# Kernel tuning notes

Measured on AMD Instinct MI355X. Metric: run time of the kernel, lower is better.

Reference implementation:

```python
import jax, jax.numpy as jnp
import numpy as np

N = 100000
E = 800000
IN_DIM = 128
H = 4
D = 32
HD = H * D  # 128
EPS = 1e-5
NEG_SLOPE = 0.2


def setup_inputs() -> dict:
    key = jax.random.key(0)
    ks = jax.random.split(key, 12)
    feat = jax.random.normal(ks[0], (N, IN_DIM), dtype=jnp.float32)
    src = jax.random.randint(ks[1], (E,), 0, N)
    dst = jax.random.randint(ks[2], (E,), 0, N)
    s = 1.0 / np.sqrt(IN_DIM)
    W_src = jax.random.uniform(ks[3], (HD, IN_DIM), jnp.float32, -s, s)
    b_src = jax.random.uniform(ks[4], (HD,), jnp.float32, -s, s)
    attn_l = jax.random.normal(ks[5], (1, H, D), dtype=jnp.float32) * np.sqrt(2.0 / (H * D + 1)) * np.sqrt(2.0)
    attn_r = jax.random.normal(ks[6], (1, H, D), dtype=jnp.float32) * np.sqrt(2.0 / (H * D + 1)) * np.sqrt(2.0)
    W_skip = jax.random.uniform(ks[7], (HD, IN_DIM), jnp.float32, -s, s)
    b_skip = jax.random.uniform(ks[8], (HD,), jnp.float32, -s, s)
    sg = 1.0 / np.sqrt(3 * HD)
    W_gate = jax.random.uniform(ks[9], (1, 3 * HD), jnp.float32, -sg, sg)
    b_gate = jax.random.uniform(ks[10], (1,), jnp.float32, -sg, sg)
    ln_g = jnp.ones((HD,), jnp.float32)
    ln_b = jnp.zeros((HD,), jnp.float32)
    prelu_a = jnp.full((1,), 0.25, jnp.float32)
    return {"feat": feat, "src": src, "dst": dst, "W_src": W_src, "b_src": b_src,
            "attn_l": attn_l, "attn_r": attn_r, "W_skip": W_skip, "b_skip": b_skip,
            "W_gate": W_gate, "b_gate": b_gate, "ln_g": ln_g, "ln_b": ln_b,
            "prelu_a": prelu_a}


def reference(feat, src, dst, W_src, b_src, attn_l, attn_r, W_skip, b_skip,
              W_gate, b_gate, ln_g, ln_b, prelu_a):
    # node projection -> [N, H, D]
    feat_src = (feat @ W_src.T + b_src).reshape(N, H, D)
    el = jnp.sum(feat_src * attn_l, axis=-1)  # [N, H]
    er = jnp.sum(feat_src * attn_r, axis=-1)  # [N, H]
    # per-edge logits with leaky relu
    e = el[src] + er[dst]                      # [E, H]
    e = jnp.where(e >= 0, e, NEG_SLOPE * e)
    # edge softmax over incoming edges of each dst node
    emax = jax.ops.segment_max(e, dst, num_segments=N)   # [N, H]
    ex = jnp.exp(e - emax[dst])                          # [E, H]
    esum = jax.ops.segment_sum(ex, dst, num_segments=N)  # [N, H]
    a = ex / esum[dst]                                   # [E, H]
    # weighted aggregation: sum_e a_e * ft[src_e]
    m = feat_src[src] * a[:, :, None]                    # [E, H, D]
    rst = jax.ops.segment_sum(m, dst, num_segments=N).reshape(N, HD)
    # gated skip connection
    skip = feat @ W_skip.T + b_skip                      # [N, HD]
    g_in = jnp.concatenate([rst, skip, rst - skip], axis=-1)
    gate = jax.nn.sigmoid(g_in @ W_gate.T + b_gate)      # [N, 1]
    rst = gate * rst + (1.0 - gate) * skip
    # layer norm
    mu = jnp.mean(rst, axis=-1, keepdims=True)
    var = jnp.var(rst, axis=-1, keepdims=True)
    y = (rst - mu) / jnp.sqrt(var + EPS) * ln_g + ln_b
    # PReLU (single shared alpha)
    return jnp.where(y >= 0, y, prelu_a[0] * y)
```

## Files before the change

### kernel.cpp

```cpp
#include <hip/hip_runtime.h>

typedef __attribute__((ext_vector_type(8))) short short8;
typedef __attribute__((ext_vector_type(4))) float v4f;

__device__ __forceinline__ ushort f2bf(float x) {
    unsigned u = __float_as_uint(x);
    u = u + 0x7fffu + ((u >> 16) & 1u);
    return (ushort)(u >> 16);
}
__device__ __forceinline__ float bflo(unsigned u) { return __uint_as_float(u << 16); }
__device__ __forceinline__ float bfhi(unsigned u) { return __uint_as_float(u & 0xffff0000u); }

#define CPAD 16
#define SLOT 32
#define GGRID 512
#define CHSZ 4096

__global__ __launch_bounds__(256) void k_edges(
    const int* __restrict__ src, const int* __restrict__ dst,
    int* __restrict__ counts_p, int* __restrict__ padcsr,
    int E_, int ns8, int n)
{
    const int slice = blockIdx.x & 7;
    const int chunk = blockIdx.x >> 3;
    const int lo = slice * ns8;
    int hi = lo + ns8; if (hi > n) hi = n;
    const unsigned span = (unsigned)(hi - lo);

    int cend = (chunk + 1) * CHSZ; if (cend > E_) cend = E_;
    for (int off = chunk * CHSZ + threadIdx.x * 4; off < cend; off += 1024) {
        if (off + 4 <= cend) {
            int4 d4 = *(const int4*)(dst + off);
            int4 s4 = *(const int4*)(src + off);
            if ((unsigned)(d4.x - lo) < span) {
                int r = atomicAdd(&counts_p[(size_t)d4.x * CPAD], 1);
                if (r < SLOT) padcsr[(size_t)d4.x * SLOT + r] = s4.x;
            }
            if ((unsigned)(d4.y - lo) < span) {
                int r = atomicAdd(&counts_p[(size_t)d4.y * CPAD], 1);
                if (r < SLOT) padcsr[(size_t)d4.y * SLOT + r] = s4.y;
            }
            if ((unsigned)(d4.z - lo) < span) {
                int r = atomicAdd(&counts_p[(size_t)d4.z * CPAD], 1);
                if (r < SLOT) padcsr[(size_t)d4.z * SLOT + r] = s4.z;
            }
            if ((unsigned)(d4.w - lo) < span) {
                int r = atomicAdd(&counts_p[(size_t)d4.w * CPAD], 1);
                if (r < SLOT) padcsr[(size_t)d4.w * SLOT + r] = s4.w;
            }
        } else {
            for (int q = off; q < cend; ++q) {
                int d = dst[q];
                if ((unsigned)(d - lo) < span) {
                    int r = atomicAdd(&counts_p[(size_t)d * CPAD], 1);
                    if (r < SLOT) padcsr[(size_t)d * SLOT + r] = src[q];
                }
            }
        }
    }
}

__global__ __launch_bounds__(256, 2) void k_gemm(
    const float* __restrict__ feat, const float* __restrict__ Wsrc,
    const float* __restrict__ Wskip,
    const float* __restrict__ bsrc, const float* __restrict__ bskip,
    const float* __restrict__ attn_l, const float* __restrict__ attn_r,
    ushort* __restrict__ feat_src, ushort* __restrict__ skip_bf,
    float* __restrict__ el, float* __restrict__ er, int n)
{
    __shared__ float sA[8192];
    const int tid = threadIdx.x;
    const int wave = tid >> 6, lane = tid & 63;
    const int quad = lane >> 4, l16 = lane & 15;
    const int n0 = wave * 64;
    const int ntile = (n + 31) >> 5;

    short8 bb[4][4];
    #pragma unroll
    for (int nt = 0; nt < 4; ++nt) {
        int r = n0 + l16 + nt * 16;
        const float* wr = (r < 128) ? (Wsrc + (size_t)r * 128)
                                    : (Wskip + (size_t)(r - 128) * 128);
        #pragma unroll
        for (int k = 0; k < 4; ++k) {
            float4 w0 = *(const float4*)(wr + quad * 8 + k * 32);
            float4 w1 = *(const float4*)(wr + quad * 8 + k * 32 + 4);
            short8 v;
            v[0] = (short)f2bf(w0.x); v[1] = (short)f2bf(w0.y);
            v[2] = (short)f2bf(w0.z); v[3] = (short)f2bf(w0.w);
            v[4] = (short)f2bf(w1.x); v[5] = (short)f2bf(w1.y);
            v[6] = (short)f2bf(w1.z); v[7] = (short)f2bf(w1.w);
            bb[nt][k] = v;
            asm volatile("" : "+v"(bb[nt][k]));
        }
    }

    float4 bias[4], al[4], ar[4];
    #pragma unroll
    for (int nt = 0; nt < 4; ++nt) {
        int cb = n0 + nt * 16 + quad * 4;
        bias[nt] = (n0 < 128) ? *(const float4*)(bsrc + cb)
                              : *(const float4*)(bskip + (cb - 128));
        al[nt] = *(const float4*)(attn_l + (cb & 127));
        ar[nt] = *(const float4*)(attn_r + (cb & 127));
    }

    const int trow = tid >> 5;
    const int scb  = ((tid & 31) * 16) ^ ((trow & 7) << 4);
    const char* gbase = (const char*)feat;

    auto stage = [&](int tt, int buf) {
        #pragma unroll
        for (int i = 0; i < 4; ++i) {
            int grow = tt * 32 + i * 8 + trow;
            if (grow > n - 1) grow = n - 1;
            const void* g = gbase + (size_t)grow * 512 + scb;
            float* lp = sA + buf * 4096 + i * 1024 + wave * 256;
            __builtin_amdgcn_global_load_lds(
                (const __attribute__((address_space(1))) void*)g,
                (__attribute__((address_space(3))) void*)lp, 16, 0, 0);
        }
    };

    int t = blockIdx.x;
    if (t >= ntile) return;
    stage(t, 0);
    int p = 0;
    bool first = true;

    for (; t < ntile; t += GGRID) {
        int tn = t + GGRID;
        bool pre = (tn < ntile);
        if (pre) stage(tn, p ^ 1);
        if (!pre)       asm volatile("s_waitcnt vmcnt(0)" ::: "memory");
        else if (first) asm volatile("s_waitcnt vmcnt(4)" ::: "memory");
        else            asm volatile("s_waitcnt vmcnt(8)" ::: "memory");
        first = false;
        __builtin_amdgcn_s_barrier();
        __builtin_amdgcn_sched_barrier(0);

        const int row0 = t * 32;
        v4f acc[2][4] = {};
        const char* sAB = (const char*)sA + p * 16384;
        const int sw = (l16 & 7) << 4;
        #pragma unroll
        for (int k = 0; k < 4; ++k) {
            int c = quad * 32 + k * 128;
            float4 f0 = *(const float4*)(sAB + l16 * 512 + ((c     ) ^ sw));
            float4 f1 = *(const float4*)(sAB + l16 * 512 + ((c + 16) ^ sw));
            float4 g0 = *(const float4*)(sAB + (l16 + 16) * 512 + ((c     ) ^ sw));
            float4 g1 = *(const float4*)(sAB + (l16 + 16) * 512 + ((c + 16) ^ sw));
            short8 a0, a1;
            a0[0] = (short)f2bf(f0.x); a0[1] = (short)f2bf(f0.y);
            a0[2] = (short)f2bf(f0.z); a0[3] = (short)f2bf(f0.w);
            a0[4] = (short)f2bf(f1.x); a0[5] = (short)f2bf(f1.y);
            a0[6] = (short)f2bf(f1.z); a0[7] = (short)f2bf(f1.w);
            a1[0] = (short)f2bf(g0.x); a1[1] = (short)f2bf(g0.y);
            a1[2] = (short)f2bf(g0.z); a1[3] = (short)f2bf(g0.w);
            a1[4] = (short)f2bf(g1.x); a1[5] = (short)f2bf(g1.y);
            a1[6] = (short)f2bf(g1.z); a1[7] = (short)f2bf(g1.w);
            #pragma unroll
            for (int nt = 0; nt < 4; ++nt) {
                acc[0][nt] = __builtin_amdgcn_mfma_f32_16x16x32_bf16(
                    bb[nt][k], a0, acc[0][nt], 0, 0, 0);
                acc[1][nt] = __builtin_amdgcn_mfma_f32_16x16x32_bf16(
                    bb[nt][k], a1, acc[1][nt], 0, 0, 0);
            }
        }

        #pragma unroll
        for (int nt = 0; nt < 4; ++nt) {
            #pragma unroll
            for (int mt = 0; mt < 2; ++mt) {
                acc[mt][nt][0] += bias[nt].x;
                acc[mt][nt][1] += bias[nt].y;
                acc[mt][nt][2] += bias[nt].z;
                acc[mt][nt][3] += bias[nt].w;
            }
        }

        #pragma unroll
        for (int mt = 0; mt < 2; ++mt) {
            int row = row0 + mt * 16 + l16;
            if (row < n) {
                #pragma unroll
                for (int nt = 0; nt < 4; ++nt) {
                    int cb = n0 + nt * 16 + quad * 4;
                    unsigned lo = (unsigned)f2bf(acc[mt][nt][0]) |
                                  ((unsigned)f2bf(acc[mt][nt][1]) << 16);
                    unsigned hi = (unsigned)f2bf(acc[mt][nt][2]) |
                                  ((unsigned)f2bf(acc[mt][nt][3]) << 16);
                    uint2 pv = make_uint2(lo, hi);
                    if (n0 < 128) *(uint2*)(feat_src + (size_t)row * 128 + cb) = pv;
                    else          *(uint2*)(skip_bf  + (size_t)row * 128 + (cb - 128)) = pv;
                }
            }
        }

        if (wave < 2) {
            const int hb = n0 >> 5;
            #pragma unroll
            for (int mt = 0; mt < 2; ++mt) {
                float pl0 = 0.f, pl1 = 0.f, pr0 = 0.f, pr1 = 0.f;
                #pragma unroll
                for (int i = 0; i < 4; ++i) {
                    float a0v = acc[mt][0][i], a1v = acc[mt][1][i];
                    float a2v = acc[mt][2][i], a3v = acc[mt][3][i];
                    const float* pal0 = (const float*)&al[0]; const float* pal1 = (const float*)&al[1];
                    const float* pal2 = (const float*)&al[2]; const float* pal3 = (const float*)&al[3];
                    const float* par0 = (const float*)&ar[0]; const float* par1 = (const float*)&ar[1];
                    const float* par2 = (const float*)&ar[2]; const float* par3 = (const float*)&ar[3];
                    pl0 = fmaf(a0v, pal0[i], fmaf(a1v, pal1[i], pl0));
                    pl1 = fmaf(a2v, pal2[i], fmaf(a3v, pal3[i], pl1));
                    pr0 = fmaf(a0v, par0[i], fmaf(a1v, par1[i], pr0));
                    pr1 = fmaf(a2v, par2[i], fmaf(a3v, par3[i], pr1));
                }
                pl0 += __shfl_xor(pl0, 16); pl0 += __shfl_xor(pl0, 32);
                pl1 += __shfl_xor(pl1, 16); pl1 += __shfl_xor(pl1, 32);
                pr0 += __shfl_xor(pr0, 16); pr0 += __shfl_xor(pr0, 32);
                pr1 += __shfl_xor(pr1, 16); pr1 += __shfl_xor(pr1, 32);
                int row = row0 + mt * 16 + l16;
                if (lane < 16 && row < n) {
                    *(float2*)(el + (size_t)row * 4 + hb) = make_float2(pl0, pl1);
                    *(float2*)(er + (size_t)row * 4 + hb) = make_float2(pr0, pr1);
                }
            }
        }

        __builtin_amdgcn_s_barrier();
        p ^= 1;
    }
}

__global__ __launch_bounds__(256) void k3_fused(
    const int* __restrict__ counts_p, const int* __restrict__ padcsr,
    const float* __restrict__ el, const float* __restrict__ er,
    const ushort* __restrict__ feat_src, const ushort* __restrict__ skip_bf,
    const float* __restrict__ Wg, const float* __restrict__ bg,
    const float* __restrict__ lng, const float* __restrict__ lnb,
    const float* __restrict__ pa, float* __restrict__ out, int n)
{
    int node = blockIdx.x * 8 + (threadIdx.x >> 5);
    if (node >= n) return;
    int l32 = threadIdx.x & 31;
    int j = l32 * 4;
    int h = l32 >> 3;

    int cnt = counts_p[(size_t)node * CPAD];
    if (cnt > SLOT) cnt = SLOT;
    int beg = node * SLOT, end = beg + cnt;
    float er_h = er[(size_t)node * 4 + h];
    const ushort* fbase = feat_src + j;

    float ac0 = 0.f, ac1 = 0.f, ac2 = 0.f, ac3 = 0.f;
    float bc0 = 0.f, bc1 = 0.f, bc2 = 0.f, bc3 = 0.f;
    float wsA = 0.f, wsB = 0.f;

    for (int p0 = beg; p0 < end; p0 += 32) {
        int pv = p0 + l32;
        int sv = padcsr[pv < end ? pv : end - 1];
        int cb = end - p0; if (cb > 32) cb = 32;
        for (int i = 0; i < cb; i += 4) {
            int s0 = __shfl(sv, i, 32),     s1 = __shfl(sv, i + 1, 32);
            int s2 = __shfl(sv, i + 2, 32), s3 = __shfl(sv, i + 3, 32);
            float e0 = el[(size_t)s0 * 4 + h], e1 = el[(size_t)s1 * 4 + h];
            float e2 = el[(size_t)s2 * 4 + h], e3 = el[(size_t)s3 * 4 + h];
            uint2 u0 = *(const uint2*)(fbase + (size_t)s0 * 128);
            uint2 u1 = *(const uint2*)(fbase + (size_t)s1 * 128);
            uint2 u2 = *(const uint2*)(fbase + (size_t)s2 * 128);
            uint2 u3 = *(const uint2*)(fbase + (size_t)s3 * 128);
            float t0 = e0 + er_h, t1 = e1 + er_h, t2 = e2 + er_h, t3 = e3 + er_h;
            float w0 = __expf(fmaxf(t0, 0.2f * t0));
            float w1 = (i + 1 < cb) ? __expf(fmaxf(t1, 0.2f * t1)) : 0.f;
            float w2 = (i + 2 < cb) ? __expf(fmaxf(t2, 0.2f * t2)) : 0.f;
            float w3 = (i + 3 < cb) ? __expf(fmaxf(t3, 0.2f * t3)) : 0.f;
            wsA += w0 + w2; wsB += w1 + w3;
            ac0 = fmaf(w0, bflo(u0.x), fmaf(w2, bflo(u2.x), ac0));
            ac1 = fmaf(w0, bfhi(u0.x), fmaf(w2, bfhi(u2.x), ac1));
            ac2 = fmaf(w0, bflo(u0.y), fmaf(w2, bflo(u2.y), ac2));
            ac3 = fmaf(w0, bfhi(u0.y), fmaf(w2, bfhi(u2.y), ac3));
            bc0 = fmaf(w1, bflo(u1.x), fmaf(w3, bflo(u3.x), bc0));
            bc1 = fmaf(w1, bfhi(u1.x), fmaf(w3, bfhi(u3.x), bc1));
            bc2 = fmaf(w1, bflo(u1.y), fmaf(w3, bflo(u3.y), bc2));
            bc3 = fmaf(w1, bfhi(u1.y), fmaf(w3, bfhi(u3.y), bc3));
        }
    }
    float wsum = wsA + wsB;
    float inv = (wsum > 0.f) ? 1.f / wsum : 0.f;
    float r0 = (ac0 + bc0) * inv, r1 = (ac1 + bc1) * inv;
    float r2 = (ac2 + bc2) * inv, r3 = (ac3 + bc3) * inv;

    uint2 su = *(const uint2*)(skip_bf + (size_t)node * 128 + j);
    float s0 = bflo(su.x), s1 = bfhi(su.x), s2 = bflo(su.y), s3 = bfhi(su.y);

    float4 wg0 = *(const float4*)(Wg + j);
    float4 wg1 = *(const float4*)(Wg + 128 + j);
    float4 wg2 = *(const float4*)(Wg + 256 + j);
    float g = r0 * wg0.x + s0 * wg1.x + (r0 - s0) * wg2.x
            + r1 * wg0.y + s1 * wg1.y + (r1 - s1) * wg2.y
            + r2 * wg0.z + s2 * wg1.z + (r2 - s2) * wg2.z
            + r3 * wg0.w + s3 * wg1.w + (r3 - s3) * wg2.w;
    #pragma unroll
    for (int m = 1; m < 32; m <<= 1) g += __shfl_xor(g, m, 32);
    float gate = 1.f / (1.f + __expf(-(g + bg[0])));

    float x0 = gate * r0 + (1.f - gate) * s0;
    float x1 = gate * r1 + (1.f - gate) * s1;
    float x2 = gate * r2 + (1.f - gate) * s2;
    float x3 = gate * r3 + (1.f - gate) * s3;

    float sm = (x0 + x1) + (x2 + x3);
    float sq = (x0 * x0 + x1 * x1) + (x2 * x2 + x3 * x3);
    #pragma unroll
    for (int m = 1; m < 32; m <<= 1) {
        sm += __shfl_xor(sm, m, 32);
        sq += __shfl_xor(sq, m, 32);
    }
    float mu = sm * (1.f / 128.f);
    float var = sq * (1.f / 128.f) - mu * mu;
    float rs = rsqrtf(var + 1e-5f);
    float alpha = pa[0];
    float4 lg = *(const float4*)(lng + j);
    float4 lb = *(const float4*)(lnb + j);
    float y0 = (x0 - mu) * rs * lg.x + lb.x;
    float y1 = (x1 - mu) * rs * lg.y + lb.y;
    float y2 = (x2 - mu) * rs * lg.z + lb.z;
    float y3 = (x3 - mu) * rs * lg.w + lb.w;
    y0 = y0 >= 0.f ? y0 : alpha * y0;
    y1 = y1 >= 0.f ? y1 : alpha * y1;
    y2 = y2 >= 0.f ? y2 : alpha * y2;
    y3 = y3 >= 0.f ? y3 : alpha * y3;
    *(float4*)(out + (size_t)node * 128 + j) = make_float4(y0, y1, y2, y3);
}

extern "C" void kernel_launch(void* const* d_in, const int* in_sizes, int n_in,
                              void* d_out, int out_size, void* d_ws, size_t ws_size,
                              hipStream_t stream)
{
    const float* feat   = (const float*)d_in[0];
    const int*   src    = (const int*)d_in[1];
    const int*   dst    = (const int*)d_in[2];
    const float* Wsrc   = (const float*)d_in[3];
    const float* bsrc   = (const float*)d_in[4];
    const float* attn_l = (const float*)d_in[5];
    const float* attn_r = (const float*)d_in[6];
    const float* Wskip  = (const float*)d_in[7];
    const float* bskip  = (const float*)d_in[8];
    const float* Wg     = (const float*)d_in[9];
    const float* bg     = (const float*)d_in[10];
    const float* lng    = (const float*)d_in[11];
    const float* lnb    = (const float*)d_in[12];
    const float* pa     = (const float*)d_in[13];

    const int n = in_sizes[0] / 128;
    const int E = in_sizes[1];
    float* out = (float*)d_out;

    float*  el       = (float*)d_ws;
    float*  er       = el + (size_t)n * 4;
    ushort* feat_src = (ushort*)(er + (size_t)n * 4);
    ushort* skip_bf  = feat_src + (size_t)n * 128;
    int*    counts_p = (int*)(skip_bf + (size_t)n * 128);
    int*    padcsr   = counts_p + (size_t)n * CPAD;

    hipMemsetAsync(counts_p, 0, (size_t)n * CPAD * sizeof(int), stream);

    int ns8 = (n + 7) / 8;
    int nchunk = (E + CHSZ - 1) / CHSZ;
    k_edges<<<nchunk * 8, 256, 0, stream>>>(
        src, dst, counts_p, padcsr, E, ns8, n);

    k_gemm<<<GGRID, 256, 0, stream>>>(
        feat, Wsrc, Wskip, bsrc, bskip, attn_l, attn_r,
        feat_src, skip_bf, el, er, n);

    k3_fused<<<(n + 7) / 8, 256, 0, stream>>>(
        counts_p, padcsr, el, er, feat_src, skip_bf, Wg, bg, lng, lnb, pa, out, n);
}
```

Before: 235.2 us.

## Precompute per-edge attention weights in edge-bucketing kernel after GEMM

The edge-bucketing kernel now runs after the projection GEMM. While scattering each edge into its padded CSR slot, it computes the exp(leaky_relu(el[src]+er[dst])) weights for all four heads and stores them as bf16. The aggregation kernel then reads these weights instead of gathering el and computing the exponentials, which removes the random el gathers from the hot loop. In exchange the bucketing kernel does extra random el/er reads and writes a new weight array, and the weights lose precision from bf16 rounding.

Result: slower. 267.0 us (+13.5%).

```diff
diff --git a/kernel.cpp b/kernel.cpp
--- a/kernel.cpp
+++ b/kernel.cpp
@@ -15,50 +15,6 @@
 #define SLOT 32
 #define GGRID 512
 #define CHSZ 4096
-
-__global__ __launch_bounds__(256) void k_edges(
-    const int* __restrict__ src, const int* __restrict__ dst,
-    int* __restrict__ counts_p, int* __restrict__ padcsr,
-    int E_, int ns8, int n)
-{
-    const int slice = blockIdx.x & 7;
-    const int chunk = blockIdx.x >> 3;
-    const int lo = slice * ns8;
-    int hi = lo + ns8; if (hi > n) hi = n;
-    const unsigned span = (unsigned)(hi - lo);
-
-    int cend = (chunk + 1) * CHSZ; if (cend > E_) cend = E_;
-    for (int off = chunk * CHSZ + threadIdx.x * 4; off < cend; off += 1024) {
-        if (off + 4 <= cend) {
-            int4 d4 = *(const int4*)(dst + off);
-            int4 s4 = *(const int4*)(src + off);
-            if ((unsigned)(d4.x - lo) < span) {
-                int r = atomicAdd(&counts_p[(size_t)d4.x * CPAD], 1);
-                if (r < SLOT) padcsr[(size_t)d4.x * SLOT + r] = s4.x;
-            }
-            if ((unsigned)(d4.y - lo) < span) {
-                int r = atomicAdd(&counts_p[(size_t)d4.y * CPAD], 1);
-                if (r < SLOT) padcsr[(size_t)d4.y * SLOT + r] = s4.y;
-            }
-            if ((unsigned)(d4.z - lo) < span) {
-                int r = atomicAdd(&counts_p[(size_t)d4.z * CPAD], 1);
-                if (r < SLOT) padcsr[(size_t)d4.z * SLOT + r] = s4.z;
-            }
-            if ((unsigned)(d4.w - lo) < span) {
-                int r = atomicAdd(&counts_p[(size_t)d4.w * CPAD], 1);
-                if (r < SLOT) padcsr[(size_t)d4.w * SLOT + r] = s4.w;
-            }
-        } else {
-            for (int q = off; q < cend; ++q) {
-                int d = dst[q];
-                if ((unsigned)(d - lo) < span) {
-                    int r = atomicAdd(&counts_p[(size_t)d * CPAD], 1);
-                    if (r < SLOT) padcsr[(size_t)d * SLOT + r] = src[q];
-                }
-            }
-        }
-    }
-}
 
 __global__ __launch_bounds__(256, 2) void k_gemm(
     const float* __restrict__ feat, const float* __restrict__ Wsrc,
@@ -232,9 +188,55 @@
     }
 }
 
+__global__ __launch_bounds__(256) void k_edges(
+    const int* __restrict__ src, const int* __restrict__ dst,
+    const float* __restrict__ el, const float* __restrict__ er,
+    int* __restrict__ counts_p, int* __restrict__ padcsr,
+    ushort* __restrict__ padw, int E_, int ns8, int n)
+{
+    const int slice = blockIdx.x & 7;
+    const int chunk = blockIdx.x >> 3;
+    const int lo = slice * ns8;
+    int hi = lo + ns8; if (hi > n) hi = n;
+    const unsigned span = (unsigned)(hi - lo);
+
+    auto doEdge = [&](int d, int s) {
+        if ((unsigned)(d - lo) < span) {
+            int r = atomicAdd(&counts_p[(size_t)d * CPAD], 1);
+            if (r < SLOT) {
+                padcsr[(size_t)d * SLOT + r] = s;
+                float4 e4 = *(const float4*)(el + (size_t)s * 4);
+                float4 r4 = *(const float4*)(er + (size_t)d * 4);
+                float t0 = e4.x + r4.x, t1 = e4.y + r4.y;
+                float t2 = e4.z + r4.z, t3 = e4.w + r4.w;
+                ushort4 w;
+                w.x = f2bf(__expf(fmaxf(t0, 0.2f * t0)));
+                w.y = f2bf(__expf(fmaxf(t1, 0.2f * t1)));
+                w.z = f2bf(__expf(fmaxf(t2, 0.2f * t2)));
+                w.w = f2bf(__expf(fmaxf(t3, 0.2f * t3)));
+                *(ushort4*)(padw + ((size_t)d * SLOT + r) * 4) = w;
+            }
+        }
+    };
+
+    int cend = (chunk + 1) * CHSZ; if (cend > E_) cend = E_;
+    for (int off = chunk * CHSZ + threadIdx.x * 4; off < cend; off += 1024) {
+        if (off + 4 <= cend) {
+            int4 d4 = *(const int4*)(dst + off);
+            int4 s4 = *(const int4*)(src + off);
+            doEdge(d4.x, s4.x);
+            doEdge(d4.y, s4.y);
+            doEdge(d4.z, s4.z);
+            doEdge(d4.w, s4.w);
+        } else {
+            for (int q = off; q < cend; ++q) doEdge(dst[q], src[q]);
+        }
+    }
+}
+
 __global__ __launch_bounds__(256) void k3_fused(
     const int* __restrict__ counts_p, const int* __restrict__ padcsr,
-    const float* __restrict__ el, const float* __restrict__ er,
+    const ushort* __restrict__ padw,
     const ushort* __restrict__ feat_src, const ushort* __restrict__ skip_bf,
     const float* __restrict__ Wg, const float* __restrict__ bg,
     const float* __restrict__ lng, const float* __restrict__ lnb,
@@ -249,8 +251,8 @@
     int cnt = counts_p[(size_t)node * CPAD];
     if (cnt > SLOT) cnt = SLOT;
     int beg = node * SLOT, end = beg + cnt;
-    float er_h = er[(size_t)node * 4 + h];
     const ushort* fbase = feat_src + j;
+    const ushort* wbase = padw + (size_t)node * (SLOT * 4) + h;
 
     float ac0 = 0.f, ac1 = 0.f, ac2 = 0.f, ac3 = 0.f;
     float bc0 = 0.f, bc1 = 0.f, bc2 = 0.f, bc3 = 0.f;
@@ -260,20 +262,18 @@
         int pv = p0 + l32;
         int sv = padcsr[pv < end ? pv : end - 1];
         int cb = end - p0; if (cb > 32) cb = 32;
+        int ib = p0 - beg;
         for (int i = 0; i < cb; i += 4) {
+            float w0 = bflo((unsigned)wbase[(ib + i) * 4]);
+            float w1 = (i + 1 < cb) ? bflo((unsigned)wbase[(ib + i + 1) * 4]) : 0.f;
+            float w2 = (i + 2 < cb) ? bflo((unsigned)wbase[(ib + i + 2) * 4]) : 0.f;
+            float w3 = (i + 3 < cb) ? bflo((unsigned)wbase[(ib + i + 3) * 4]) : 0.f;
             int s0 = __shfl(sv, i, 32),     s1 = __shfl(sv, i + 1, 32);
             int s2 = __shfl(sv, i + 2, 32), s3 = __shfl(sv, i + 3, 32);
-            float e0 = el[(size_t)s0 * 4 + h], e1 = el[(size_t)s1 * 4 + h];
-            float e2 = el[(size_t)s2 * 4 + h], e3 = el[(size_t)s3 * 4 + h];
             uint2 u0 = *(const uint2*)(fbase + (size_t)s0 * 128);
             uint2 u1 = *(const uint2*)(fbase + (size_t)s1 * 128);
             uint2 u2 = *(const uint2*)(fbase + (size_t)s2 * 128);
             uint2 u3 = *(const uint2*)(fbase + (size_t)s3 * 128);
-            float t0 = e0 + er_h, t1 = e1 + er_h, t2 = e2 + er_h, t3 = e3 + er_h;
-            float w0 = __expf(fmaxf(t0, 0.2f * t0));
-            float w1 = (i + 1 < cb) ? __expf(fmaxf(t1, 0.2f * t1)) : 0.f;
-            float w2 = (i + 2 < cb) ? __expf(fmaxf(t2, 0.2f * t2)) : 0.f;
-            float w3 = (i + 3 < cb) ? __expf(fmaxf(t3, 0.2f * t3)) : 0.f;
             wsA += w0 + w2; wsB += w1 + w3;
             ac0 = fmaf(w0, bflo(u0.x), fmaf(w2, bflo(u2.x), ac0));
             ac1 = fmaf(w0, bfhi(u0.x), fmaf(w2, bfhi(u2.x), ac1));
@@ -362,18 +362,19 @@
     ushort* skip_bf  = feat_src + (size_t)n * 128;
     int*    counts_p = (int*)(skip_bf + (size_t)n * 128);
     int*    padcsr   = counts_p + (size_t)n * CPAD;
+    ushort* padw     = (ushort*)(padcsr + (size_t)n * SLOT);
 
     hipMemsetAsync(counts_p, 0, (size_t)n * CPAD * sizeof(int), stream);
+
+    k_gemm<<<GGRID, 256, 0, stream>>>(
+        feat, Wsrc, Wskip, bsrc, bskip, attn_l, attn_r,
+        feat_src, skip_bf, el, er, n);
 
     int ns8 = (n + 7) / 8;
     int nchunk = (E + CHSZ - 1) / CHSZ;
     k_edges<<<nchunk * 8, 256, 0, stream>>>(
-        src, dst, counts_p, padcsr, E, ns8, n);
-
-    k_gemm<<<GGRID, 256, 0, stream>>>(
-        feat, Wsrc, Wskip, bsrc, bskip, attn_l, attn_r,
-        feat_src, skip_bf, el, er, n);
+        src, dst, el, er, counts_p, padcsr, padw, E, ns8, n);
 
     k3_fused<<<(n + 7) / 8, 256, 0, stream>>>(
-        counts_p, padcsr, el, er, feat_src, skip_bf, Wg, bg, lng, lnb, pa, out, n);
-}
+        counts_p, padcsr, padw, feat_src, skip_bf, Wg, bg, lng, lnb, pa, out, n);
+}
```
